# Kernel optimization log

Hardware: AMD Instinct MI355X
Metric: run time of the kernel (lower is better)

Reference implementation:

```python
import jax, jax.numpy as jnp
import numpy as np

N = 100000      # nodes
E = 1600000     # graph edges
P = 800000      # hypergraph incidence pairs
HE = 20000      # hyperedges
F_IN = 128      # node features
DIM = 64        # hidden dim (hard-coded in module)
NC = 40         # num_classes


def _lin_init(key, fan_in, fan_out):
    k1, k2 = jax.random.split(key)
    s = 1.0 / np.sqrt(fan_in)
    W = jax.random.uniform(k1, (fan_in, fan_out), jnp.float32, -s, s)
    b = jax.random.uniform(k2, (fan_out,), jnp.float32, -s, s)
    return W, b


def setup_inputs() -> dict:
    key = jax.random.key(0)
    ks = jax.random.split(key, 10)
    x = jax.random.normal(ks[0], (N, F_IN), jnp.float32)
    edge_index = jax.random.randint(ks[1], (2, E), 0, N, dtype=jnp.int64)
    node_idx = jax.random.randint(ks[2], (P,), 0, N, dtype=jnp.int64)
    he_idx = jax.random.randint(ks[3], (P,), 0, HE, dtype=jnp.int64)
    hyperedge_index = jnp.stack([node_idx, he_idx], axis=0)
    W_h1, b_h1 = _lin_init(ks[4], F_IN, DIM)
    W_h2, b_h2 = _lin_init(ks[5], DIM, DIM)
    W_c1, b_c1 = _lin_init(ks[6], F_IN + DIM, DIM)
    W_c2, b_c2 = _lin_init(ks[7], DIM, NC)
    W_lp, b_lp = _lin_init(ks[8], NC, NC)
    return dict(x=x, edge_index=edge_index, hyperedge_index=hyperedge_index,
                W_h1=W_h1, b_h1=b_h1, W_h2=W_h2, b_h2=b_h2,
                W_c1=W_c1, b_c1=b_c1, W_c2=W_c2, b_c2=b_c2,
                W_lp=W_lp, b_lp=b_lp)


def hypergraph_conv(x, node_idx, he_idx, W, b):
    # PyG HypergraphConv (no attention, hyperedge_weight = 1):
    # out = D^{-1} H B^{-1} H^T (x W) + b
    xw = x @ W                                    # [N, D]
    ones = jnp.ones(node_idx.shape[0], xw.dtype)
    Dn = jax.ops.segment_sum(ones, node_idx, num_segments=N)   # node degree
    Bh = jax.ops.segment_sum(ones, he_idx, num_segments=HE)    # hyperedge size
    D_inv = jnp.where(Dn > 0, 1.0 / Dn, 0.0)
    B_inv = jnp.where(Bh > 0, 1.0 / Bh, 0.0)
    # node -> hyperedge: m_e = (1/|e|) sum_{i in e} xw[i]
    msg1 = xw[node_idx] * B_inv[he_idx][:, None]               # [P, D]
    e_feat = jax.ops.segment_sum(msg1, he_idx, num_segments=HE)
    # hyperedge -> node: out_i = (1/deg(i)) sum_{e ni i} m_e
    msg2 = e_feat[he_idx] * D_inv[node_idx][:, None]           # [P, D]
    out = jax.ops.segment_sum(msg2, node_idx, num_segments=N)
    return out + b


def gcn_conv(x, edge_index, W, b):
    # PyG GCNConv: add self-loops, symmetric normalization
    xw = x @ W                                    # [N, D]
    loop = jnp.arange(N, dtype=edge_index.dtype)
    src = jnp.concatenate([edge_index[0], loop])
    dst = jnp.concatenate([edge_index[1], loop])
    deg = jax.ops.segment_sum(jnp.ones(dst.shape[0], xw.dtype), dst, num_segments=N)
    dis = jnp.where(deg > 0, jax.lax.rsqrt(deg), 0.0)
    norm = dis[src] * dis[dst]                    # [E+N]
    out = jax.ops.segment_sum(xw[src] * norm[:, None], dst, num_segments=N)
    return out + b


def reference(x, edge_index, hyperedge_index,
              W_h1, b_h1, W_h2, b_h2, W_c1, b_c1, W_c2, b_c2, W_lp, b_lp):
    node_idx, he_idx = hyperedge_index[0], hyperedge_index[1]
    x_hyper = jax.nn.relu(hypergraph_conv(x, node_idx, he_idx, W_h1, b_h1))
    # dropout is identity in eval mode
    x_hyper = hypergraph_conv(x_hyper, node_idx, he_idx, W_h2, b_h2)
    xc = jnp.concatenate([x, x_hyper], axis=1)    # [N, F_IN + DIM]
    x_gnn = jax.nn.relu(gcn_conv(xc, edge_index, W_c1, b_c1))
    x_gnn = gcn_conv(x_gnn, edge_index, W_c2, b_c2)
    return x_gnn @ W_lp + b_lp                     # [N, NC]
```

## Files before the change

kernel.cpp:

```cpp
#include <hip/hip_runtime.h>
#include <hip/hip_bf16.h>


__device__ __forceinline__ float ldf(const void* p, int f32, long long i) {
    if (f32) return ((const float*)p)[i];
    unsigned v = ((unsigned)((const unsigned short*)p)[i]) << 16;
    return __uint_as_float(v);
}

__device__ __forceinline__ int ldi(const int* __restrict__ w, int i64, long long i, int lim) {
    int v = i64 ? w[2 * i] : w[i];
    return ((unsigned)v < (unsigned)lim) ? v : 0;
}

__device__ __forceinline__ float b2f(unsigned short u) {
    return __uint_as_float(((unsigned)u) << 16);
}
__device__ __forceinline__ unsigned short f2b(float f) {
    __hip_bfloat16 h = __float2bfloat16(f);
    return *reinterpret_cast<unsigned short*>(&h);
}
__device__ __forceinline__ float4 b2f4(ushort4 u) {
    return make_float4(b2f(u.x), b2f(u.y), b2f(u.z), b2f(u.w));
}
__device__ __forceinline__ ushort4 f2b4(float4 v) {
    ushort4 u; u.x = f2b(v.x); u.y = f2b(v.y); u.z = f2b(v.z); u.w = f2b(v.w);
    return u;
}

struct DPtrs { const void* p[13]; int n[13]; };

__global__ void detect_k(DPtrs dp, int* __restrict__ flags) {
    int b = blockIdx.x;
    __shared__ int cnt;
    if (threadIdx.x == 0) cnt = 0;
    __syncthreads();
    int c = 0;
    if (b < 11) {
        const unsigned short* u = (const unsigned short*)dp.p[b];
        int np = dp.n[b]; if (np > 2048) np = 2048;
        for (int i = threadIdx.x; i < np; i += blockDim.x) {
            unsigned e = (u[i] >> 7) & 0xFFu;
            if (e != 0u && (e < 90u || e > 160u)) c++;
        }
        atomicAdd(&cnt, c);
        __syncthreads();
        if (threadIdx.x == 0) flags[b] = (cnt * 8 > np) ? 1 : 0;
    } else {
        const int* w = (const int*)dp.p[b];
        int np = dp.n[b]; if (np > 1024) np = 1024;
        for (int i = threadIdx.x; i < np; i += blockDim.x)
            if (w[2 * i + 1] != 0) c++;
        atomicAdd(&cnt, c);
        __syncthreads();
        if (threadIdx.x == 0) flags[b] = (cnt == 0) ? 1 : 0;
    }
}

struct Item { int b1; unsigned p1; int b2; unsigned p2; };

__device__ __forceinline__ Item decode(const int* __restrict__ ew, const int* __restrict__ hw,
                                       const int* __restrict__ FL, long long i,
                                       int E, int P, int N, int HE, int shN, int shH) {
    Item it; it.b2 = -1; it.p2 = 0;
    if (i < E) {
        int g = FL[11];
        int key = ldi(ew, g, (long long)E + i, N);
        int val = ldi(ew, g, i, N);
        it.b1 = key >> shN;
        it.p1 = ((unsigned)(key & ((1 << shN) - 1)) << 20) | (unsigned)val;
    } else {
        long long j = i - E;
        int g = FL[12];
        int nd = ldi(hw, g, j, N);
        int he = ldi(hw, g, (long long)P + j, HE);
        it.b1 = 256 + (nd >> shN);
        it.p1 = ((unsigned)(nd & ((1 << shN) - 1)) << 20) | (unsigned)he;
        it.b2 = 512 + (he >> shH);
        it.p2 = ((unsigned)(he & ((1 << shH) - 1)) << 20) | (unsigned)nd;
    }
    return it;
}

__global__ void bucket_count_k(const int* __restrict__ ew, const int* __restrict__ hw,
                               const int* __restrict__ FL, int* __restrict__ gcnt,
                               int E, int P, int N, int HE, int shN, int shH) {
    __shared__ int hist[768];
    int t = threadIdx.x;
    for (int b = t; b < 768; b += 256) hist[b] = 0;
    __syncthreads();
    long long T = (long long)E + P;
    long long stride = (long long)gridDim.x * 256;
    for (long long i = (long long)blockIdx.x * 256 + t; i < T; i += stride) {
        Item it = decode(ew, hw, FL, i, E, P, N, HE, shN, shH);
        atomicAdd(&hist[it.b1], 1);
        if (it.b2 >= 0) atomicAdd(&hist[it.b2], 1);
    }
    __syncthreads();
    for (int b = t; b < 768; b += 256) {
        int h = hist[b];
        if (h) atomicAdd(&gcnt[b], h);
    }
}

__global__ void bucket_scan_k(const int* __restrict__ gcnt, int* __restrict__ bkOff,
                              int* __restrict__ gcur, int E, int P) {
    __shared__ int sh[256];
    int t = threadIdx.x;
    long long rbase[3] = {0, (long long)E, (long long)E + P};
    for (int c = 0; c < 3; c++) {
        int v = gcnt[c * 256 + t];
        sh[t] = v;
        __syncthreads();
        for (int o = 1; o < 256; o <<= 1) {
            int y = (t >= o) ? sh[t - o] : 0;
            __syncthreads();
            sh[t] += y;
            __syncthreads();
        }
        int excl = sh[t] - v;
        bkOff[c * 256 + t] = excl;
        gcur[c * 256 + t] = (int)(rbase[c] + excl);
        __syncthreads();
    }
}

#define PCHUNK 8192

__global__ void bucket_place_k(const int* __restrict__ ew, const int* __restrict__ hw,
                               const int* __restrict__ FL, int* __restrict__ gcur,
                               unsigned* __restrict__ pbuf,
                               int E, int P, int N, int HE, int shN, int shH) {
    __shared__ int hist[768];
    __shared__ int cur[768];
    long long T = (long long)E + P;
    long long start = (long long)blockIdx.x * PCHUNK;
    long long end = start + PCHUNK; if (end > T) end = T;
    int t = threadIdx.x;
    for (int b = t; b < 768; b += 256) hist[b] = 0;
    __syncthreads();
    for (long long i = start + t; i < end; i += 256) {
        Item it = decode(ew, hw, FL, i, E, P, N, HE, shN, shH);
        atomicAdd(&hist[it.b1], 1);
        if (it.b2 >= 0) atomicAdd(&hist[it.b2], 1);
    }
    __syncthreads();
    for (int b = t; b < 768; b += 256) {
        int h = hist[b];
        cur[b] = h ? atomicAdd(&gcur[b], h) : 0;
    }
    __syncthreads();
    for (long long i = start + t; i < end; i += 256) {
        Item it = decode(ew, hw, FL, i, E, P, N, HE, shN, shH);
        int s1 = atomicAdd(&cur[it.b1], 1);
        pbuf[s1] = it.p1;
        if (it.b2 >= 0) {
            int s2 = atomicAdd(&cur[it.b2], 1);
            pbuf[s2] = it.p2;
        }
    }
}

__global__ void build_k(const unsigned* __restrict__ pbuf,
                        const int* __restrict__ gcnt, const int* __restrict__ bkOff,
                        int* __restrict__ eoff, int* __restrict__ ecnt, int* __restrict__ esrc,
                        int* __restrict__ poffN, int* __restrict__ pcntN, int* __restrict__ pheL,
                        int* __restrict__ poffH, int* __restrict__ pcntH, int* __restrict__ pniL,
                        int E, int P, int N, int HE, int shN, int shH) {
    __shared__ int hist[512];
    __shared__ int offs[512];
    __shared__ int s2[256];
    int b = blockIdx.x, t = threadIdx.x;
    int csr = b >> 8, lb = b & 255;
    int sh    = (csr == 2) ? shH : shN;
    int nkeys = (csr == 2) ? HE : N;
    int span = 1 << sh;
    int keyBase = lb << sh;
    if (keyBase >= nkeys) return;
    int keyEnd = keyBase + span; if (keyEnd > nkeys) keyEnd = nkeys;
    int cnt = gcnt[b];
    long long rbase = (csr == 0) ? 0 : ((csr == 1) ? (long long)E : (long long)E + P);
    long long pstart = rbase + bkOff[b];
    int lstBase = bkOff[b];
    int* off  = (csr == 0) ? eoff : ((csr == 1) ? poffN : poffH);
    int* cntA = (csr == 0) ? ecnt : ((csr == 1) ? pcntN : pcntH);
    int* lst  = (csr == 0) ? esrc : ((csr == 1) ? pheL : pniL);

    for (int k = t; k < 512; k += 256) hist[k] = 0;
    __syncthreads();
    for (int i = t; i < cnt; i += 256)
        atomicAdd(&hist[pbuf[pstart + i] >> 20], 1);
    __syncthreads();
    int a0 = hist[2 * t], a1 = hist[2 * t + 1];
    s2[t] = a0 + a1;
    __syncthreads();
    for (int o = 1; o < 256; o <<= 1) {
        int y = (t >= o) ? s2[t - o] : 0;
        __syncthreads();
        s2[t] += y;
        __syncthreads();
    }
    int excl = s2[t] - (a0 + a1);
    offs[2 * t] = excl;
    offs[2 * t + 1] = excl + a0;
    __syncthreads();
    for (int k = keyBase + t; k < keyEnd; k += 256) {
        off[k]  = lstBase + offs[k - keyBase];
        cntA[k] = hist[k - keyBase];
    }
    __syncthreads();
    for (int i = t; i < cnt; i += 256) {
        unsigned u = pbuf[pstart + i];
        int lk = u >> 20;
        int slot = atomicAdd(&offs[lk], 1);
        lst[lstBase + slot] = (int)(u & 0xFFFFFu);
    }
}

__global__ void norms_k(const int* __restrict__ ecnt, const int* __restrict__ pcntN,
                        const int* __restrict__ pcntH, float* __restrict__ dis,
                        float* __restrict__ Dinv, float* __restrict__ Binv, int N, int HE) {
    int i = blockIdx.x * blockDim.x + threadIdx.x;
    if (i < N) dis[i] = rsqrtf((float)(ecnt[i] + 1));
    else if (i < 2 * N) { int c = pcntN[i - N]; Dinv[i - N] = c ? (1.f / (float)c) : 0.f; }
    else if (i < 2 * N + HE) { int c = pcntH[i - 2 * N]; Binv[i - 2 * N] = c ? (1.f / (float)c) : 0.f; }
}

__global__ void wlp2_k(const void* Wc2, const int* fWc2, const void* Wlp, const int* fWlp,
                       const void* bc2, const int* fbc2, const void* blp, const int* fblp,
                       float* __restrict__ Wlp2, float* __restrict__ bias2, int NC) {
    extern __shared__ float sm[];
    float* sW2 = sm;
    float* sLP = sm + 64 * NC;
    int t = threadIdx.x;
    int fw2 = fWc2[0], flp = fWlp[0];
    for (int e = t; e < 64 * NC; e += blockDim.x) sW2[e] = ldf(Wc2, fw2, e);
    for (int e = t; e < NC * NC; e += blockDim.x) sLP[e] = ldf(Wlp, flp, e);
    __syncthreads();
    for (int e = t; e < 64 * NC; e += blockDim.x) {
        int r = e / NC, c = e % NC;
        float s = 0.f;
        for (int k = 0; k < NC; k++) s = fmaf(sW2[r * NC + k], sLP[k * NC + c], s);
        Wlp2[e] = s;
    }
    if (t < NC) {
        float s = ldf(blp, fblp[0], t);
        int fb2 = fbc2[0];
        for (int k = 0; k < NC; k++) s = fmaf(ldf(bc2, fb2, k), sLP[k * NC + t], s);
        bias2[t] = s;
    }
}

__global__ void gat_n2e_k(const ushort4* __restrict__ xw, const int* __restrict__ off,
                          const int* __restrict__ cnt, const int* __restrict__ lst,
                          const float* __restrict__ Binv, ushort4* __restrict__ ef, int HE) {
    int idx = blockIdx.x * blockDim.x + threadIdx.x;
    int e = idx >> 4, l = idx & 15;
    if (e >= HE) return;
    int o = off[e], c = cnt[e];
    float4 a = make_float4(0.f, 0.f, 0.f, 0.f);
    int j = 0;
    for (; j + 4 <= c; j += 4) {
        int s0 = lst[o + j], s1 = lst[o + j + 1], s2 = lst[o + j + 2], s3 = lst[o + j + 3];
        float4 v0 = b2f4(xw[((long long)s0 << 4) + l]);
        float4 v1 = b2f4(xw[((long long)s1 << 4) + l]);
        float4 v2 = b2f4(xw[((long long)s2 << 4) + l]);
        float4 v3 = b2f4(xw[((long long)s3 << 4) + l]);
        a.x += (v0.x + v1.x) + (v2.x + v3.x);
        a.y += (v0.y + v1.y) + (v2.y + v3.y);
        a.z += (v0.z + v1.z) + (v2.z + v3.z);
        a.w += (v0.w + v1.w) + (v2.w + v3.w);
    }
    for (; j < c; j++) {
        float4 v = b2f4(xw[((long long)lst[o + j] << 4) + l]);
        a.x += v.x; a.y += v.y; a.z += v.z; a.w += v.w;
    }
    float bi = Binv[e];
    a.x *= bi; a.y *= bi; a.z *= bi; a.w *= bi;
    ef[((long long)e << 4) + l] = f2b4(a);
}

template <bool RELU>
__global__ void gat_e2n_k(const ushort4* __restrict__ ef, const int* __restrict__ off,
                          const int* __restrict__ cnt, const int* __restrict__ lst,
                          const float* __restrict__ Dinv, const void* __restrict__ bias,
                          const int* __restrict__ fb, ushort4* __restrict__ out, int N) {
    int idx = blockIdx.x * blockDim.x + threadIdx.x;
    int w = idx >> 4, l = idx & 15;
    if (w >= N) return;
    int o = off[w], c = cnt[w];
    float4 a = make_float4(0.f, 0.f, 0.f, 0.f);
    int j = 0;
    for (; j + 4 <= c; j += 4) {
        int s0 = lst[o + j], s1 = lst[o + j + 1], s2 = lst[o + j + 2], s3 = lst[o + j + 3];
        float4 v0 = b2f4(ef[((long long)s0 << 4) + l]);
        float4 v1 = b2f4(ef[((long long)s1 << 4) + l]);
        float4 v2 = b2f4(ef[((long long)s2 << 4) + l]);
        float4 v3 = b2f4(ef[((long long)s3 << 4) + l]);
        a.x += (v0.x + v1.x) + (v2.x + v3.x);
        a.y += (v0.y + v1.y) + (v2.y + v3.y);
        a.z += (v0.z + v1.z) + (v2.z + v3.z);
        a.w += (v0.w + v1.w) + (v2.w + v3.w);
    }
    for (; j < c; j++) {
        float4 v = b2f4(ef[((long long)lst[o + j] << 4) + l]);
        a.x += v.x; a.y += v.y; a.z += v.z; a.w += v.w;
    }
    float di = Dinv[w];
    int fbv = fb[0];
    float4 b = make_float4(ldf(bias, fbv, 4 * l), ldf(bias, fbv, 4 * l + 1),
                           ldf(bias, fbv, 4 * l + 2), ldf(bias, fbv, 4 * l + 3));
    a.x = a.x * di + b.x; a.y = a.y * di + b.y;
    a.z = a.z * di + b.z; a.w = a.w * di + b.w;
    if (RELU) {
        a.x = fmaxf(a.x, 0.f); a.y = fmaxf(a.y, 0.f);
        a.z = fmaxf(a.z, 0.f); a.w = fmaxf(a.w, 0.f);
    }
    out[((long long)w << 4) + l] = f2b4(a);
}

template <bool RELU>
__global__ void gcn_gat_k(const ushort4* __restrict__ y, const int* __restrict__ off,
                          const int* __restrict__ cnt, const int* __restrict__ lst,
                          const float* __restrict__ dis, const void* __restrict__ bias,
                          const int* __restrict__ fb, ushort4* __restrict__ out, int N) {
    int idx = blockIdx.x * blockDim.x + threadIdx.x;
    int w = idx >> 4, l = idx & 15;
    if (w >= N) return;
    int o = off[w], c = cnt[w];
    float4 a = b2f4(y[((long long)w << 4) + l]);
    int j = 0;
    for (; j + 4 <= c; j += 4) {
        int s0 = lst[o + j], s1 = lst[o + j + 1], s2 = lst[o + j + 2], s3 = lst[o + j + 3];
        float4 v0 = b2f4(y[((long long)s0 << 4) + l]);
        float4 v1 = b2f4(y[((long long)s1 << 4) + l]);
        float4 v2 = b2f4(y[((long long)s2 << 4) + l]);
        float4 v3 = b2f4(y[((long long)s3 << 4) + l]);
        a.x += (v0.x + v1.x) + (v2.x + v3.x);
        a.y += (v0.y + v1.y) + (v2.y + v3.y);
        a.z += (v0.z + v1.z) + (v2.z + v3.z);
        a.w += (v0.w + v1.w) + (v2.w + v3.w);
    }
    for (; j < c; j++) {
        float4 v = b2f4(y[((long long)lst[o + j] << 4) + l]);
        a.x += v.x; a.y += v.y; a.z += v.z; a.w += v.w;
    }
    float dd = dis[w];
    int fbv = fb[0];
    float4 b = make_float4(ldf(bias, fbv, 4 * l), ldf(bias, fbv, 4 * l + 1),
                           ldf(bias, fbv, 4 * l + 2), ldf(bias, fbv, 4 * l + 3));
    a.x = a.x * dd + b.x; a.y = a.y * dd + b.y;
    a.z = a.z * dd + b.z; a.w = a.w * dd + b.w;
    if (RELU) {
        a.x = fmaxf(a.x, 0.f); a.y = fmaxf(a.y, 0.f);
        a.z = fmaxf(a.z, 0.f); a.w = fmaxf(a.w, 0.f);
    }
    out[((long long)w << 4) + l] = f2b4(a);
}

__global__ void gcn_gatM_k(const ushort4* __restrict__ y2, const int* __restrict__ off,
                           const int* __restrict__ cnt, const int* __restrict__ lst,
                           const float* __restrict__ dis, const float* __restrict__ bias2,
                           float4* __restrict__ out4, int N, int nc4, int npw) {
    int idx = blockIdx.x * blockDim.x + threadIdx.x;
    int wave = idx >> 6, l64 = idx & 63;
    int grp = l64 / 10, li = l64 - grp * 10;
    if (nc4 != 10) { grp = l64 / nc4; li = l64 - grp * nc4; }
    int w = wave * npw + grp;
    if (grp >= npw || w >= N) return;
    int o = off[w], c = cnt[w];
    float4 a = b2f4(y2[(long long)w * nc4 + li]);
    int j = 0;
    for (; j + 4 <= c; j += 4) {
        int s0 = lst[o + j], s1 = lst[o + j + 1], s2 = lst[o + j + 2], s3 = lst[o + j + 3];
        float4 v0 = b2f4(y2[(long long)s0 * nc4 + li]);
        float4 v1 = b2f4(y2[(long long)s1 * nc4 + li]);
        float4 v2 = b2f4(y2[(long long)s2 * nc4 + li]);
        float4 v3 = b2f4(y2[(long long)s3 * nc4 + li]);
        a.x += (v0.x + v1.x) + (v2.x + v3.x);
        a.y += (v0.y + v1.y) + (v2.y + v3.y);
        a.z += (v0.z + v1.z) + (v2.z + v3.z);
        a.w += (v0.w + v1.w) + (v2.w + v3.w);
    }
    for (; j < c; j++) {
        float4 v = b2f4(y2[(long long)lst[o + j] * nc4 + li]);
        a.x += v.x; a.y += v.y; a.z += v.z; a.w += v.w;
    }
    float dd = dis[w];
    float4 b = *(const float4*)&bias2[4 * li];
    a.x = a.x * dd + b.x; a.y = a.y * dd + b.y;
    a.z = a.z * dd + b.z; a.w = a.w * dd + b.w;
    out4[(long long)w * nc4 + li] = a;
}

template <bool ABF16>
__device__ __forceinline__ float4 loadA4(const void* A, int af, long long base) {
    if constexpr (ABF16) {
        return b2f4(*(const ushort4*)((const unsigned short*)A + base));
    } else {
        if (af) return *(const float4*)((const float*)A + base);
        float4 v;
        v.x = ldf(A, 0, base); v.y = ldf(A, 0, base + 1);
        v.z = ldf(A, 0, base + 2); v.w = ldf(A, 0, base + 3);
        return v;
    }
}

template <bool ABF16, bool SCALE>
__global__ __launch_bounds__(256)
void gemm64_k(const void* __restrict__ A, const int* __restrict__ fA,
              const void* __restrict__ B, const int* __restrict__ fB,
              const float* __restrict__ dscale,
              unsigned short* __restrict__ C, int NR, int K, int M) {
    const int af = fA ? fA[0] : 1;
    const int bf = fB ? fB[0] : 1;
    __shared__ float As[16][68];
    __shared__ float Bs[16][68];
    const int t = threadIdx.x;
    const int tx = t & 15, ty = t >> 4;
    const long long m0 = (long long)blockIdx.x * 64;
    float c[4][4] = {};
    for (int k0 = 0; k0 < K; k0 += 16) {
        {
            int row = t >> 2;
            int kk = (t & 3) * 4;
            long long r = m0 + row;
            float4 v = make_float4(0.f, 0.f, 0.f, 0.f);
            if (r < NR) v = loadA4<ABF16>(A, af, r * K + k0 + kk);
            As[kk + 0][row] = v.x; As[kk + 1][row] = v.y;
            As[kk + 2][row] = v.z; As[kk + 3][row] = v.w;
        }
        {
            int krow = t >> 4;
            int nn = (t & 15) * 4;
            int k = k0 + krow;
            float4 v = make_float4(0.f, 0.f, 0.f, 0.f);
            if (nn < M) {
                long long base = (long long)k * M + nn;
                if (bf) v = *(const float4*)((const float*)B + base);
                else {
                    v.x = ldf(B, 0, base); v.y = ldf(B, 0, base + 1);
                    v.z = ldf(B, 0, base + 2); v.w = ldf(B, 0, base + 3);
                }
            }
            *(float4*)&Bs[krow][nn] = v;
        }
        __syncthreads();
#pragma unroll
        for (int k = 0; k < 16; k++) {
            float4 a = *(const float4*)&As[k][ty * 4];
            float4 b = *(const float4*)&Bs[k][tx * 4];
            float av[4] = {a.x, a.y, a.z, a.w};
            float bv[4] = {b.x, b.y, b.z, b.w};
#pragma unroll
            for (int i = 0; i < 4; i++)
#pragma unroll
                for (int j = 0; j < 4; j++) c[i][j] = fmaf(av[i], bv[j], c[i][j]);
        }
        __syncthreads();
    }
    int n = tx * 4;
    if (n < M) {
#pragma unroll
        for (int i = 0; i < 4; i++) {
            long long r = m0 + ty * 4 + i;
            if (r < NR) {
                float s = SCALE ? dscale[r] : 1.f;
                long long o = r * M + n;
                *(ushort4*)&C[o] = f2b4(make_float4(c[i][0] * s, c[i][1] * s,
                                                    c[i][2] * s, c[i][3] * s));
            }
        }
    }
}

__global__ __launch_bounds__(256)
void gemm64cat_k(const void* __restrict__ A, const int* __restrict__ fA,
                 const unsigned short* __restrict__ A2,
                 const void* __restrict__ B, const int* __restrict__ fB,
                 const float* __restrict__ dscale,
                 unsigned short* __restrict__ C, int NR, int M) {
    const int af = fA ? fA[0] : 1;
    const int bf = fB ? fB[0] : 1;
    __shared__ float As[16][68];
    __shared__ float Bs[16][68];
    const int t = threadIdx.x;
    const int tx = t & 15, ty = t >> 4;
    const long long m0 = (long long)blockIdx.x * 64;
    float c[4][4] = {};
    for (int k0 = 0; k0 < 192; k0 += 16) {
        {
            int row = t >> 2;
            int kk = (t & 3) * 4;
            long long r = m0 + row;
            float4 v = make_float4(0.f, 0.f, 0.f, 0.f);
            if (r < NR) {
                if (k0 < 128) v = loadA4<false>(A, af, r * 128 + k0 + kk);
                else v = b2f4(*(const ushort4*)&A2[r * 64 + (k0 - 128) + kk]);
            }
            As[kk + 0][row] = v.x; As[kk + 1][row] = v.y;
            As[kk + 2][row] = v.z; As[kk + 3][row] = v.w;
        }
        {
            int krow = t >> 4;
            int nn = (t & 15) * 4;
            int k = k0 + krow;
            float4 v;
            long long base = (long long)k * M + nn;
            if (bf) v = *(const float4*)((const float*)B + base);
            else {
                v.x = ldf(B, 0, base); v.y = ldf(B, 0, base + 1);
                v.z = ldf(B, 0, base + 2); v.w = ldf(B, 0, base + 3);
            }
            *(float4*)&Bs[krow][nn] = v;
        }
        __syncthreads();
#pragma unroll
        for (int k = 0; k < 16; k++) {
            float4 a = *(const float4*)&As[k][ty * 4];
            float4 b = *(const float4*)&Bs[k][tx * 4];
            float av[4] = {a.x, a.y, a.z, a.w};
            float bv[4] = {b.x, b.y, b.z, b.w};
#pragma unroll
            for (int i = 0; i < 4; i++)
#pragma unroll
                for (int j = 0; j < 4; j++) c[i][j] = fmaf(av[i], bv[j], c[i][j]);
        }
        __syncthreads();
    }
    int n = tx * 4;
#pragma unroll
    for (int i = 0; i < 4; i++) {
        long long r = m0 + ty * 4 + i;
        if (r < NR) {
            float s = dscale[r];
            long long o = r * M + n;
            *(ushort4*)&C[o] = f2b4(make_float4(c[i][0] * s, c[i][1] * s,
                                                c[i][2] * s, c[i][3] * s));
        }
    }
}

static inline dim3 g1d(long long n, int b) { return dim3((unsigned)((n + b - 1) / b)); }
static inline int imin(int a, int b) { return a < b ? a : b; }

extern "C" void kernel_launch(void* const* d_in, const int* in_sizes, int n_in,
                              void* d_out, int out_size, void* d_ws, size_t ws_size,
                              hipStream_t stream) {
    const int N  = in_sizes[0] / 128;
    const int E  = in_sizes[1] / 2;
    const int P  = in_sizes[2] / 2;
    const int HE = 20000;
    const int NC = in_sizes[9] / 64;
    const int nc4 = NC / 4;
    const int npw = 64 / nc4;

    const void* x    = d_in[0];
    const int*  ew   = (const int*)d_in[1];
    const int*  hw   = (const int*)d_in[2];
    const void* W_h1 = d_in[3];
    const void* b_h1 = d_in[4];
    const void* W_h2 = d_in[5];
    const void* b_h2 = d_in[6];
    const void* W_c1 = d_in[7];
    const void* b_c1 = d_in[8];
    const void* W_c2 = d_in[9];
    const void* b_c2 = d_in[10];
    const void* W_lp = d_in[11];
    const void* b_lp = d_in[12];

    int shN = 0; while (((N - 1) >> shN) >= 256) shN++;
    int shH = 0; while (((HE - 1) >> shH) >= 256) shH++;

    char* wp = (char*)d_ws;
    auto allocF = [&](size_t n) { float* p = (float*)wp; wp += n * 4; return p; };
    auto allocI = [&](size_t n) { int* p = (int*)wp; wp += n * 4; return p; };
    unsigned short* ub  = (unsigned short*)allocF((size_t)N * 32);
    unsigned short* hb  = (unsigned short*)allocF((size_t)N * 32);
    unsigned short* efb = (unsigned short*)allocF((size_t)HE * 32);
    float* dis   = allocF(N);
    float* Dinv  = allocF(N);
    float* Binv  = allocF(HE);
    float* Wlp2  = allocF((size_t)64 * NC);
    float* bias2 = allocF(NC);
    int* ecnt  = allocI(N);
    int* pcntN = allocI(N);
    int* pcntH = allocI(HE);
    int* eoff  = allocI(N);
    int* poffN = allocI(N);
    int* poffH = allocI(HE);
    int* esrc  = allocI(E);
    int* pheL  = allocI(P);
    int* pniL  = allocI(P);
    int* gBkt  = allocI(768);
    int* bkOff = allocI(768);
    int* gcur  = allocI(768);
    int* FL    = allocI(16);
    unsigned* pbuf = (unsigned*)allocI((size_t)E + 2 * (size_t)P);

    dim3 b256(256), d1(1);

    DPtrs dp;
    const void* farr[11] = {x, W_h1, b_h1, W_h2, b_h2, W_c1, b_c1, W_c2, b_c2, W_lp, b_lp};
    const int   fsz[11]  = {in_sizes[0], in_sizes[3], in_sizes[4], in_sizes[5], in_sizes[6],
                            in_sizes[7], in_sizes[8], in_sizes[9], in_sizes[10], in_sizes[11],
                            in_sizes[12]};
    for (int i = 0; i < 11; ++i) { dp.p[i] = farr[i]; dp.n[i] = fsz[i]; }
    dp.p[11] = ew; dp.n[11] = imin(E, 1024);
    dp.p[12] = hw; dp.n[12] = imin(P, 1024);
    detect_k<<<dim3(13), b256, 0, stream>>>(dp, FL);
    const int* fX   = FL + 0;
    const int* fWh1 = FL + 1,  *fbh1 = FL + 2;
    const int* fWh2 = FL + 3,  *fbh2 = FL + 4;
    const int* fWc1 = FL + 5,  *fbc1 = FL + 6;
    const int* fWc2 = FL + 7,  *fbc2 = FL + 8;
    const int* fWlp = FL + 9,  *fblp = FL + 10;

    hipMemsetAsync(gBkt, 0, 768 * 4, stream);
    bucket_count_k<<<dim3(512), b256, 0, stream>>>(ew, hw, FL, gBkt, E, P, N, HE, shN, shH);
    bucket_scan_k<<<d1, b256, 0, stream>>>(gBkt, bkOff, gcur, E, P);
    {
        long long T = (long long)E + P;
        int nChunks = (int)((T + PCHUNK - 1) / PCHUNK);
        bucket_place_k<<<dim3(nChunks), b256, 0, stream>>>(ew, hw, FL, gcur, pbuf,
                                                           E, P, N, HE, shN, shH);
    }
    build_k<<<dim3(768), b256, 0, stream>>>(pbuf, gBkt, bkOff,
                                            eoff, ecnt, esrc,
                                            poffN, pcntN, pheL,
                                            poffH, pcntH, pniL,
                                            E, P, N, HE, shN, shH);

    norms_k<<<g1d(2 * N + HE, 256), b256, 0, stream>>>(ecnt, pcntN, pcntH, dis, Dinv, Binv, N, HE);
    wlp2_k<<<d1, b256, (64 * NC + NC * NC) * 4, stream>>>(
        W_c2, fWc2, W_lp, fWlp, b_c2, fbc2, b_lp, fblp, Wlp2, bias2, NC);

    const dim3 gemmGrid((N + 63) / 64);
    const dim3 gatN16(g1d((long long)N * 16, 256));
    const dim3 gatH16(g1d((long long)HE * 16, 256));
    const dim3 gatNC(g1d((long long)((N + npw - 1) / npw) * 64, 256));

    gemm64_k<false, false><<<gemmGrid, b256, 0, stream>>>(x, fX, W_h1, fWh1, nullptr, ub, N, 128, 64);
    gat_n2e_k<<<gatH16, b256, 0, stream>>>((const ushort4*)ub, poffH, pcntH, pniL, Binv, (ushort4*)efb, HE);
    gat_e2n_k<true><<<gatN16, b256, 0, stream>>>((const ushort4*)efb, poffN, pcntN, pheL, Dinv, b_h1, fbh1, (ushort4*)hb, N);

    gemm64_k<true, false><<<gemmGrid, b256, 0, stream>>>(hb, nullptr, W_h2, fWh2, nullptr, ub, N, 64, 64);
    gat_n2e_k<<<gatH16, b256, 0, stream>>>((const ushort4*)ub, poffH, pcntH, pniL, Binv, (ushort4*)efb, HE);
    gat_e2n_k<false><<<gatN16, b256, 0, stream>>>((const ushort4*)efb, poffN, pcntN, pheL, Dinv, b_h2, fbh2, (ushort4*)hb, N);

    gemm64cat_k<<<gemmGrid, b256, 0, stream>>>(x, fX, hb, W_c1, fWc1, dis, ub, N, 64);
    gcn_gat_k<true><<<gatN16, b256, 0, stream>>>((const ushort4*)ub, eoff, ecnt, esrc, dis, b_c1, fbc1, (ushort4*)hb, N);

    gemm64_k<true, true><<<gemmGrid, b256, 0, stream>>>(hb, nullptr, Wlp2, nullptr, dis, ub, N, 64, NC);
    gcn_gatM_k<<<gatNC, b256, 0, stream>>>((const ushort4*)ub, eoff, ecnt, esrc, dis, bias2, (float4*)d_out, N, nc4, npw);
}
```

Baseline: 497.1 us.

## Replace scalar FMA GEMMs with bf16 MFMA kernels and halve bucket chunk size

The four dense GEMM kernels, previously fp32 FMA with a 4x4 register tile, become MFMA 16x16x32 bf16 kernels. Each block stages its whole 64-row A tile and the transposed weight matrix in LDS as bf16, then each wave computes 16 rows across NF 16-wide column fragments. Inputs now round to bf16 before multiply, which adds precision loss on x. The weight transpose is reloaded per block with scalar strided loads and outputs are written as scalar bf16 stores. The bucket placement chunk size is also halved to raise parallelism.

```diff
diff --git a/kernel.cpp b/kernel.cpp
--- a/kernel.cpp
+++ b/kernel.cpp
@@ -1,6 +1,9 @@
 #include <hip/hip_runtime.h>
 #include <hip/hip_bf16.h>
 
+
+typedef short bf16x8 __attribute__((ext_vector_type(8)));
+typedef float f32x4v __attribute__((ext_vector_type(4)));
 
 __device__ __forceinline__ float ldf(const void* p, int f32, long long i) {
     if (f32) return ((const float*)p)[i];
@@ -125,7 +128,7 @@
     }
 }
 
-#define PCHUNK 8192
+#define PCHUNK 4096
 
 __global__ void bucket_place_k(const int* __restrict__ ew, const int* __restrict__ hw,
                                const int* __restrict__ FL, int* __restrict__ gcur,
@@ -393,150 +396,129 @@
     out4[(long long)w * nc4 + li] = a;
 }
 
-template <bool ABF16>
-__device__ __forceinline__ float4 loadA4(const void* A, int af, long long base) {
-    if constexpr (ABF16) {
-        return b2f4(*(const ushort4*)((const unsigned short*)A + base));
-    } else {
-        if (af) return *(const float4*)((const float*)A + base);
-        float4 v;
-        v.x = ldf(A, 0, base); v.y = ldf(A, 0, base + 1);
-        v.z = ldf(A, 0, base + 2); v.w = ldf(A, 0, base + 3);
-        return v;
-    }
-}
-
-template <bool ABF16, bool SCALE>
+template <int NF, bool ABF16, bool SCALE>
 __global__ __launch_bounds__(256)
-void gemm64_k(const void* __restrict__ A, const int* __restrict__ fA,
-              const void* __restrict__ B, const int* __restrict__ fB,
-              const float* __restrict__ dscale,
-              unsigned short* __restrict__ C, int NR, int K, int M) {
+void mfma_gemm_k(const void* __restrict__ A, const int* __restrict__ fA,
+                 const void* __restrict__ B, const int* __restrict__ fB,
+                 const float* __restrict__ dscale,
+                 unsigned short* __restrict__ C, int NR, int K, int M) {
+    extern __shared__ unsigned short sm16[];
+    const int KP = K + 8;
+    unsigned short* As = sm16;
+    unsigned short* Wt = sm16 + 64 * KP;
+    const int t = threadIdx.x;
     const int af = fA ? fA[0] : 1;
     const int bf = fB ? fB[0] : 1;
-    __shared__ float As[16][68];
-    __shared__ float Bs[16][68];
+    const long long m0 = (long long)blockIdx.x * 64;
+
+    for (int idx = t * 4; idx < 64 * K; idx += 1024) {
+        int row = idx / K, col = idx - row * K;
+        long long r = m0 + row;
+        ushort4 o = make_ushort4(0, 0, 0, 0);
+        if (r < NR) {
+            long long base = r * (long long)K + col;
+            if (ABF16 || !af) o = *(const ushort4*)((const unsigned short*)A + base);
+            else o = f2b4(*(const float4*)((const float*)A + base));
+        }
+        *(ushort4*)&As[row * KP + col] = o;
+    }
+    for (int e = t; e < NF * 16 * K; e += 256) {
+        int n = e / K, k = e - n * K;
+        float v = (n < M) ? ldf(B, bf, (long long)k * M + n) : 0.f;
+        Wt[n * KP + k] = f2b(v);
+    }
+    __syncthreads();
+
+    const int w = t >> 6, l = t & 63;
+    const int m = l & 15, q = l >> 4;
+    f32x4v acc[NF];
+#pragma unroll
+    for (int f = 0; f < NF; f++) acc[f] = (f32x4v){0.f, 0.f, 0.f, 0.f};
+
+    const int aBase = (w * 16 + m) * KP + q * 8;
+    for (int k0 = 0; k0 < K; k0 += 32) {
+        bf16x8 afr = *(const bf16x8*)&As[aBase + k0];
+#pragma unroll
+        for (int f = 0; f < NF; f++) {
+            bf16x8 bfr = *(const bf16x8*)&Wt[(f * 16 + m) * KP + q * 8 + k0];
+            acc[f] = __builtin_amdgcn_mfma_f32_16x16x32_bf16(afr, bfr, acc[f], 0, 0, 0);
+        }
+    }
+
+#pragma unroll
+    for (int reg = 0; reg < 4; reg++) {
+        long long r = m0 + w * 16 + q * 4 + reg;
+        if (r < NR) {
+            float s = SCALE ? dscale[r] : 1.f;
+#pragma unroll
+            for (int f = 0; f < NF; f++) {
+                int col = f * 16 + m;
+                if (col < M) C[r * (long long)M + col] = f2b(acc[f][reg] * s);
+            }
+        }
+    }
+}
+
+__global__ __launch_bounds__(256)
+void mfma_gemmcat_k(const void* __restrict__ A, const int* __restrict__ fA,
+                    const unsigned short* __restrict__ A2,
+                    const void* __restrict__ B, const int* __restrict__ fB,
+                    const float* __restrict__ dscale,
+                    unsigned short* __restrict__ C, int NR, int M) {
+    extern __shared__ unsigned short sm16[];
+    const int K = 192, KP = 200;
+    unsigned short* As = sm16;
+    unsigned short* Wt = sm16 + 64 * KP;
     const int t = threadIdx.x;
-    const int tx = t & 15, ty = t >> 4;
-    const long long m0 = (long long)blockIdx.x * 64;
-    float c[4][4] = {};
-    for (int k0 = 0; k0 < K; k0 += 16) {
-        {
-            int row = t >> 2;
-            int kk = (t & 3) * 4;
-            long long r = m0 + row;
-            float4 v = make_float4(0.f, 0.f, 0.f, 0.f);
-            if (r < NR) v = loadA4<ABF16>(A, af, r * K + k0 + kk);
-            As[kk + 0][row] = v.x; As[kk + 1][row] = v.y;
-            As[kk + 2][row] = v.z; As[kk + 3][row] = v.w;
-        }
-        {
-            int krow = t >> 4;
-            int nn = (t & 15) * 4;
-            int k = k0 + krow;
-            float4 v = make_float4(0.f, 0.f, 0.f, 0.f);
-            if (nn < M) {
-                long long base = (long long)k * M + nn;
-                if (bf) v = *(const float4*)((const float*)B + base);
-                else {
-                    v.x = ldf(B, 0, base); v.y = ldf(B, 0, base + 1);
-                    v.z = ldf(B, 0, base + 2); v.w = ldf(B, 0, base + 3);
-                }
-            }
-            *(float4*)&Bs[krow][nn] = v;
-        }
-        __syncthreads();
-#pragma unroll
-        for (int k = 0; k < 16; k++) {
-            float4 a = *(const float4*)&As[k][ty * 4];
-            float4 b = *(const float4*)&Bs[k][tx * 4];
-            float av[4] = {a.x, a.y, a.z, a.w};
-            float bv[4] = {b.x, b.y, b.z, b.w};
-#pragma unroll
-            for (int i = 0; i < 4; i++)
-#pragma unroll
-                for (int j = 0; j < 4; j++) c[i][j] = fmaf(av[i], bv[j], c[i][j]);
-        }
-        __syncthreads();
-    }
-    int n = tx * 4;
-    if (n < M) {
-#pragma unroll
-        for (int i = 0; i < 4; i++) {
-            long long r = m0 + ty * 4 + i;
-            if (r < NR) {
-                float s = SCALE ? dscale[r] : 1.f;
-                long long o = r * M + n;
-                *(ushort4*)&C[o] = f2b4(make_float4(c[i][0] * s, c[i][1] * s,
-                                                    c[i][2] * s, c[i][3] * s));
-            }
-        }
-    }
-}
-
-__global__ __launch_bounds__(256)
-void gemm64cat_k(const void* __restrict__ A, const int* __restrict__ fA,
-                 const unsigned short* __restrict__ A2,
-                 const void* __restrict__ B, const int* __restrict__ fB,
-                 const float* __restrict__ dscale,
-                 unsigned short* __restrict__ C, int NR, int M) {
     const int af = fA ? fA[0] : 1;
     const int bf = fB ? fB[0] : 1;
-    __shared__ float As[16][68];
-    __shared__ float Bs[16][68];
-    const int t = threadIdx.x;
-    const int tx = t & 15, ty = t >> 4;
     const long long m0 = (long long)blockIdx.x * 64;
-    float c[4][4] = {};
-    for (int k0 = 0; k0 < 192; k0 += 16) {
-        {
-            int row = t >> 2;
-            int kk = (t & 3) * 4;
-            long long r = m0 + row;
-            float4 v = make_float4(0.f, 0.f, 0.f, 0.f);
-            if (r < NR) {
-                if (k0 < 128) v = loadA4<false>(A, af, r * 128 + k0 + kk);
-                else v = b2f4(*(const ushort4*)&A2[r * 64 + (k0 - 128) + kk]);
+
+    for (int idx = t * 4; idx < 64 * K; idx += 1024) {
+        int row = idx / K, col = idx - row * K;
+        long long r = m0 + row;
+        ushort4 o = make_ushort4(0, 0, 0, 0);
+        if (r < NR) {
+            if (col < 128) {
+                long long base = r * 128 + col;
+                if (!af) o = *(const ushort4*)((const unsigned short*)A + base);
+                else o = f2b4(*(const float4*)((const float*)A + base));
+            } else {
+                o = *(const ushort4*)&A2[r * 64 + (col - 128)];
             }
-            As[kk + 0][row] = v.x; As[kk + 1][row] = v.y;
-            As[kk + 2][row] = v.z; As[kk + 3][row] = v.w;
-        }
-        {
-            int krow = t >> 4;
-            int nn = (t & 15) * 4;
-            int k = k0 + krow;
-            float4 v;
-            long long base = (long long)k * M + nn;
-            if (bf) v = *(const float4*)((const float*)B + base);
-            else {
-                v.x = ldf(B, 0, base); v.y = ldf(B, 0, base + 1);
-                v.z = ldf(B, 0, base + 2); v.w = ldf(B, 0, base + 3);
-            }
-            *(float4*)&Bs[krow][nn] = v;
-        }
-        __syncthreads();
-#pragma unroll
-        for (int k = 0; k < 16; k++) {
-            float4 a = *(const float4*)&As[k][ty * 4];
-            float4 b = *(const float4*)&Bs[k][tx * 4];
-            float av[4] = {a.x, a.y, a.z, a.w};
-            float bv[4] = {b.x, b.y, b.z, b.w};
-#pragma unroll
-            for (int i = 0; i < 4; i++)
-#pragma unroll
-                for (int j = 0; j < 4; j++) c[i][j] = fmaf(av[i], bv[j], c[i][j]);
-        }
-        __syncthreads();
-    }
-    int n = tx * 4;
-#pragma unroll
-    for (int i = 0; i < 4; i++) {
-        long long r = m0 + ty * 4 + i;
+        }
+        *(ushort4*)&As[row * KP + col] = o;
+    }
+    for (int e = t; e < 64 * K; e += 256) {
+        int n = e / K, k = e - n * K;
+        Wt[n * KP + k] = f2b(ldf(B, bf, (long long)k * M + n));
+    }
+    __syncthreads();
+
+    const int w = t >> 6, l = t & 63;
+    const int m = l & 15, q = l >> 4;
+    f32x4v acc[4];
+#pragma unroll
+    for (int f = 0; f < 4; f++) acc[f] = (f32x4v){0.f, 0.f, 0.f, 0.f};
+
+    const int aBase = (w * 16 + m) * KP + q * 8;
+#pragma unroll
+    for (int k0 = 0; k0 < K; k0 += 32) {
+        bf16x8 afr = *(const bf16x8*)&As[aBase + k0];
+#pragma unroll
+        for (int f = 0; f < 4; f++) {
+            bf16x8 bfr = *(const bf16x8*)&Wt[(f * 16 + m) * KP + q * 8 + k0];
+            acc[f] = __builtin_amdgcn_mfma_f32_16x16x32_bf16(afr, bfr, acc[f], 0, 0, 0);
+        }
+    }
+#pragma unroll
+    for (int reg = 0; reg < 4; reg++) {
+        long long r = m0 + w * 16 + q * 4 + reg;
         if (r < NR) {
             float s = dscale[r];
-            long long o = r * M + n;
-            *(ushort4*)&C[o] = f2b4(make_float4(c[i][0] * s, c[i][1] * s,
-                                                c[i][2] * s, c[i][3] * s));
+#pragma unroll
+            for (int f = 0; f < 4; f++)
+                C[r * (long long)M + f * 16 + m] = f2b(acc[f][reg] * s);
         }
     }
 }
@@ -640,17 +622,25 @@
     const dim3 gatH16(g1d((long long)HE * 16, 256));
     const dim3 gatNC(g1d((long long)((N + npw - 1) / npw) * 64, 256));
 
-    gemm64_k<false, false><<<gemmGrid, b256, 0, stream>>>(x, fX, W_h1, fWh1, nullptr, ub, N, 128, 64);
+    const int lds128 = (64 + 64) * 136 * 2;
+    const int lds64a = (64 + 64) * 72 * 2;
+    const int lds64b = (64 + 48) * 72 * 2;
+    const int lds192 = (64 + 64) * 200 * 2;
+
+    mfma_gemm_k<4, false, false><<<gemmGrid, b256, lds128, stream>>>(
+        x, fX, W_h1, fWh1, nullptr, ub, N, 128, 64);
     gat_n2e_k<<<gatH16, b256, 0, stream>>>((const ushort4*)ub, poffH, pcntH, pniL, Binv, (ushort4*)efb, HE);
     gat_e2n_k<true><<<gatN16, b256, 0, stream>>>((const ushort4*)efb, poffN, pcntN, pheL, Dinv, b_h1, fbh1, (ushort4*)hb, N);
 
-    gemm64_k<true, false><<<gemmGrid, b256, 0, stream>>>(hb, nullptr, W_h2, fWh2, nullptr, ub, N, 64, 64);
+    mfma_gemm_k<4, true, false><<<gemmGrid, b256, lds64a, stream>>>(
+        hb, nullptr, W_h2, fWh2, nullptr, ub, N, 64, 64);
     gat_n2e_k<<<gatH16, b256, 0, stream>>>((const ushort4*)ub, poffH, pcntH, pniL, Binv, (ushort4*)efb, HE);
     gat_e2n_k<false><<<gatN16, b256, 0, stream>>>((const ushort4*)efb, poffN, pcntN, pheL, Dinv, b_h2, fbh2, (ushort4*)hb, N);
 
-    gemm64cat_k<<<gemmGrid, b256, 0, stream>>>(x, fX, hb, W_c1, fWc1, dis, ub, N, 64);
+    mfma_gemmcat_k<<<gemmGrid, b256, lds192, stream>>>(x, fX, hb, W_c1, fWc1, dis, ub, N, 64);
     gcn_gat_k<true><<<gatN16, b256, 0, stream>>>((const ushort4*)ub, eoff, ecnt, esrc, dis, b_c1, fbc1, (ushort4*)hb, N);
 
-    gemm64_k<true, true><<<gemmGrid, b256, 0, stream>>>(hb, nullptr, Wlp2, nullptr, dis, ub, N, 64, NC);
+    mfma_gemm_k<3, true, true><<<gemmGrid, b256, lds64b, stream>>>(
+        hb, nullptr, Wlp2, nullptr, dis, ub, N, 64, NC);
     gcn_gatM_k<<<gatNC, b256, 0, stream>>>((const ushort4*)ub, eoff, ecnt, esrc, dis, bias2, (float4*)d_out, N, nc4, npw);
 }
```

Measured after the change: 526.5 us. +5.9%, slower.
